# Kernel optimization log

Hardware: AMD Instinct MI355X
Metric: run time of the kernel (lower is better)

## Reference

```python
import jax, jax.numpy as jnp
import numpy as np

N = 50000          # total nodes
B = 10             # graphs in batch
NPG = N // B       # nodes per graph (equal-sized graphs)
E = 800000         # edges
IN_DIM = 128
HID = 128
NHEAD = 4
DHEAD = HID // NHEAD
T = 1000
SLOPE = 0.2        # leaky_relu negative slope
ALPHA_L = 2.0


def _ln(x, g=None, b=None, eps=1e-5):
    mu = jnp.mean(x, axis=-1, keepdims=True)
    var = jnp.var(x, axis=-1, keepdims=True)
    y = (x - mu) * jax.lax.rsqrt(var + eps)
    if g is not None:
        y = y * g + b
    return y


def _gatv2(h, src, dst, Ws, Wd, a, b):
    # DGL GATv2Conv, share_weights=False, residual=False, bias=True, activation=gelu
    fs = (h @ Ws).reshape(N, NHEAD, DHEAD)
    fd = (h @ Wd).reshape(N, NHEAD, DHEAD)
    # per-edge attention logits [E, NHEAD]
    e = jnp.sum(jax.nn.leaky_relu(fs[src] + fd[dst], SLOPE) * a, axis=-1)
    # edge softmax grouped by destination node
    m = jax.ops.segment_max(e, dst, num_segments=N)
    ee = jnp.exp(e - m[dst])
    den = jax.ops.segment_sum(ee, dst, num_segments=N)
    alpha = ee / den[dst]                                  # [E, NHEAD]
    rst = jax.ops.segment_sum(alpha[..., None] * fs[src], dst, num_segments=N)
    rst = jax.nn.gelu(rst + b.reshape(1, NHEAD, DHEAD), approximate=False)
    return rst.reshape(N, HID)


def _forward(x, noise, sab, somab, time_emb,
             Ws0, Wd0, a0, b0, g0, be0,
             Ws1, Wd1, a1, b1, g1, be1,
             Wo1, bo1, Wo2, bo2, src, dst, t):
    # sample_q: statistics-matched signed noise
    miu = jnp.mean(x, axis=0)
    std = jnp.std(x, axis=0, ddof=1)          # torch.std is unbiased
    nz = _ln(noise) * std + miu
    nz = jnp.sign(x) * jnp.abs(nz)
    s1 = jnp.repeat(sab[t], NPG)[:, None]
    s2 = jnp.repeat(somab[t], NPG)[:, None]
    x_t = s1 * x + s2 * nz
    temb = jnp.repeat(time_emb[t], NPG, axis=0)
    # Denoising_Unet
    h = jnp.concatenate([x_t, temb], axis=1)   # [N, IN_DIM+HID]
    h = _ln(_gatv2(h, src, dst, Ws0, Wd0, a0, b0), g0, be0)
    h_in = h
    h = _gatv2(h, src, dst, Ws1, Wd1, a1, b1)
    h = _ln(h + h_in, g1, be1)                 # residual (shapes match)
    out = jax.nn.relu(h @ Wo1 + bo1) @ Wo2 + bo2
    # loss_fn
    mse = jnp.mean((out - x) ** 2)
    on = out / jnp.maximum(jnp.linalg.norm(out, axis=-1, keepdims=True), 1e-12)
    xn = x / jnp.maximum(jnp.linalg.norm(x, axis=-1, keepdims=True), 1e-12)
    cos = jnp.mean((1.0 - jnp.sum(on * xn, axis=-1)) ** ALPHA_L)
    return mse + 0.1 * cos


def setup_inputs() -> dict:
    key = jax.random.key(0)
    ks = jax.random.split(key, 26)
    betas = np.linspace(1e-4, 0.02, T, dtype=np.float64)
    ab = np.cumprod(1.0 - betas)
    s = 0.02
    in0 = IN_DIM + HID
    inp = {}
    inp['x'] = jax.random.normal(ks[0], (N, IN_DIM), jnp.float32)
    inp['noise'] = jax.random.normal(ks[1], (N, IN_DIM), jnp.float32)
    inp['src'] = jax.random.randint(ks[2], (E,), 0, N, dtype=jnp.int32)
    inp['dst'] = jax.random.randint(ks[3], (E,), 0, N, dtype=jnp.int32)
    inp['t'] = jax.random.randint(ks[4], (B,), 0, T, dtype=jnp.int32)
    inp['sab'] = jnp.asarray(np.sqrt(ab), jnp.float32)
    inp['somab'] = jnp.asarray(np.sqrt(1.0 - ab), jnp.float32)
    inp['time_emb'] = jax.random.normal(ks[5], (T, HID), jnp.float32) * s
    inp['Ws0'] = jax.random.normal(ks[6], (in0, HID), jnp.float32) * s
    inp['Wd0'] = jax.random.normal(ks[7], (in0, HID), jnp.float32) * s
    inp['a0'] = jax.random.normal(ks[8], (NHEAD, DHEAD), jnp.float32) * s
    inp['b0'] = jnp.zeros((HID,), jnp.float32)
    inp['g0'] = jnp.ones((HID,), jnp.float32)
    inp['be0'] = jnp.zeros((HID,), jnp.float32)
    inp['Ws1'] = jax.random.normal(ks[9], (HID, HID), jnp.float32) * s
    inp['Wd1'] = jax.random.normal(ks[10], (HID, HID), jnp.float32) * s
    inp['a1'] = jax.random.normal(ks[11], (NHEAD, DHEAD), jnp.float32) * s
    inp['b1'] = jnp.zeros((HID,), jnp.float32)
    inp['g1'] = jnp.ones((HID,), jnp.float32)
    inp['be1'] = jnp.zeros((HID,), jnp.float32)
    inp['Wo1'] = jax.random.normal(ks[12], (HID, HID), jnp.float32) * s
    inp['bo1'] = jnp.zeros((HID,), jnp.float32)
    inp['Wo2'] = jax.random.normal(ks[13], (HID, IN_DIM), jnp.float32) * s
    inp['bo2'] = jnp.zeros((IN_DIM,), jnp.float32)
    return inp


def reference(x, noise, src, dst, t, sab, somab, time_emb,
              Ws0, Wd0, a0, b0, g0, be0,
              Ws1, Wd1, a1, b1, g1, be1,
              Wo1, bo1, Wo2, bo2):
    return _forward(x, noise, sab, somab, time_emb,
                    Ws0, Wd0, a0, b0, g0, be0,
                    Ws1, Wd1, a1, b1, g1, be1,
                    Wo1, bo1, Wo2, bo2, src, dst, t)
```

## Files before the change

### kernel.cpp

```cpp
#include <hip/hip_runtime.h>
#include <hip/hip_bf16.h>
#include <hip/hip_fp16.h>
#include <math.h>

#define NN 50000
#define EE 800000
#define NPG 5000

typedef short bf16x8 __attribute__((ext_vector_type(8)));
typedef float f32x4 __attribute__((ext_vector_type(4)));

__device__ __forceinline__ float gelu_exact(float v) {
    return 0.5f * v * (1.0f + erff(v * 0.70710678118654752440f));
}

__device__ __forceinline__ ushort f2b(float f) {
    union { float f; uint u; } v; v.f = f;
    uint r = (v.u + 0x7fffu + ((v.u >> 16) & 1)) >> 16;
    return (ushort)r;
}
__device__ __forceinline__ uint pack2(float a, float b) {
    return (uint)f2b(a) | ((uint)f2b(b) << 16);
}
__device__ __forceinline__ float blo(uint u) {
    union { uint u; float f; } v; v.u = u << 16; return v.f;
}
__device__ __forceinline__ float bhi(uint u) {
    union { uint u; float f; } v; v.u = u & 0xffff0000u; return v.f;
}
__device__ __forceinline__ void unpack8(uint4 u, float* f) {
    f[0] = blo(u.x); f[1] = bhi(u.x); f[2] = blo(u.y); f[3] = bhi(u.y);
    f[4] = blo(u.z); f[5] = bhi(u.z); f[6] = blo(u.w); f[7] = bhi(u.w);
}

__device__ __forceinline__ uchar f2e5m2(float v) {
    __half h = __float2half(v);
    union { __half h; ushort u; } c; c.h = h;
    return (uchar)((c.u + 0x7fu + ((c.u >> 8) & 1u)) >> 8);
}
__device__ __forceinline__ float e5m2f(uint b) {
    union { ushort u; __half h; } c; c.u = (ushort)(b << 8);
    return __half2float(c.h);
}
__device__ __forceinline__ void dec8(uint2 u, float* f) {
#pragma unroll
    for (int i = 0; i < 2; ++i) {
        uint w = (&u.x)[i];
        f[4 * i]     = e5m2f(w & 0xffu);
        f[4 * i + 1] = e5m2f((w >> 8) & 0xffu);
        f[4 * i + 2] = e5m2f((w >> 16) & 0xffu);
        f[4 * i + 3] = e5m2f((w >> 24) & 0xffu);
    }
}

__global__ __launch_bounds__(256) void head1_kernel(const float* __restrict__ x,
        float* __restrict__ sums, const int* __restrict__ dst, int* __restrict__ counts,
        const float* __restrict__ Ws0, const float* __restrict__ Wd0,
        const float* __restrict__ Ws1, const float* __restrict__ Wd1,
        const float* __restrict__ Wo1, const float* __restrict__ Wo2,
        ushort* __restrict__ Wt0, ushort* __restrict__ Wt1,
        ushort* __restrict__ Wo1t, ushort* __restrict__ Wo2t) {
    int bid = blockIdx.x;
    int tid = threadIdx.x;
    if (bid < 1024) {
        int col4 = (tid & 31) * 4;
        int rowgrp = tid >> 5;
        float s0 = 0.f, s1 = 0.f, s2 = 0.f, s3 = 0.f;
        float q0 = 0.f, q1 = 0.f, q2 = 0.f, q3 = 0.f;
        for (int r = bid * 8 + rowgrp; r < NN; r += 8192) {
            float4 v = *(const float4*)(x + (size_t)r * 128 + col4);
            s0 += v.x; s1 += v.y; s2 += v.z; s3 += v.w;
            q0 += v.x * v.x; q1 += v.y * v.y; q2 += v.z * v.z; q3 += v.w * v.w;
        }
        s0 += __shfl_xor(s0, 32); s1 += __shfl_xor(s1, 32);
        s2 += __shfl_xor(s2, 32); s3 += __shfl_xor(s3, 32);
        q0 += __shfl_xor(q0, 32); q1 += __shfl_xor(q1, 32);
        q2 += __shfl_xor(q2, 32); q3 += __shfl_xor(q3, 32);
        __shared__ float red[4][32][8];
        int wv = tid >> 6, l = tid & 63;
        if (l < 32) {
            float* p = red[wv][l];
            p[0] = s0; p[1] = s1; p[2] = s2; p[3] = s3;
            p[4] = q0; p[5] = q1; p[6] = q2; p[7] = q3;
        }
        __syncthreads();
        if (tid < 32) {
            float a0 = 0.f, a1 = 0.f, a2 = 0.f, a3 = 0.f;
            float b0 = 0.f, b1 = 0.f, b2 = 0.f, b3 = 0.f;
#pragma unroll
            for (int w = 0; w < 4; ++w) {
                float* p = red[w][tid];
                a0 += p[0]; a1 += p[1]; a2 += p[2]; a3 += p[3];
                b0 += p[4]; b1 += p[5]; b2 += p[6]; b3 += p[7];
            }
            int c = tid * 4;
            atomicAdd(&sums[c], a0); atomicAdd(&sums[c + 1], a1);
            atomicAdd(&sums[c + 2], a2); atomicAdd(&sums[c + 3], a3);
            atomicAdd(&sums[128 + c], b0); atomicAdd(&sums[128 + c + 1], b1);
            atomicAdd(&sums[128 + c + 2], b2); atomicAdd(&sums[128 + c + 3], b3);
        }
    } else if (bid < 4149) {
        int i = (bid - 1024) * 256 + tid;
        if (i < EE) atomicAdd(&counts[dst[i]], 1);
    } else {
        int i = (bid - 4149) * 256 + tid;
        if (i < 65536) {
            int c = i >> 8, k = i & 255;
            const float* W = (c < 128) ? Ws0 : Wd0;
            Wt0[c * 256 + k] = f2b(W[k * 128 + (c & 127)]);
        } else if (i < 98304) {
            int j = i - 65536;
            int c = j >> 7, k = j & 127;
            const float* W = (c < 128) ? Ws1 : Wd1;
            Wt1[c * 128 + k] = f2b(W[k * 128 + (c & 127)]);
        } else if (i < 114688) {
            int j = i - 98304;
            int c = j >> 7, k = j & 127;
            Wo1t[c * 128 + k] = f2b(Wo1[k * 128 + c]);
        } else if (i < 131072) {
            int j = i - 114688;
            int c = j >> 7, k = j & 127;
            Wo2t[c * 128 + k] = f2b(Wo2[k * 128 + c]);
        }
    }
}

__global__ __launch_bounds__(1024) void head2_kernel(const int* __restrict__ counts,
        int* __restrict__ blockSums, float* __restrict__ stats, int n) {
    int bid = blockIdx.x;
    int tid = threadIdx.x;
    if (bid < 49) {
        int i = bid * 1024 + tid;
        int v = (i < n) ? counts[i] : 0;
#pragma unroll
        for (int o = 32; o > 0; o >>= 1) v += __shfl_down(v, o);
        __shared__ int sh[16];
        int lane = tid & 63, wv = tid >> 6;
        if (lane == 0) sh[wv] = v;
        __syncthreads();
        if (tid == 0) {
            int s = 0;
#pragma unroll
            for (int k = 0; k < 16; ++k) s += sh[k];
            blockSums[bid] = s;
        }
    } else {
        if (tid < 128) {
            int c = tid;
            float sum = stats[c], sumsq = stats[128 + c];
            float mu = sum / (float)n;
            float var = (sumsq - sum * sum / (float)n) / (float)(n - 1);
            stats[256 + c] = mu;
            stats[384 + c] = sqrtf(fmaxf(var, 0.f));
        }
    }
}

__global__ __launch_bounds__(1024) void head3_kernel(const float* __restrict__ x,
        const float* __restrict__ noise, const int* __restrict__ t,
        const float* __restrict__ sab, const float* __restrict__ somab,
        const float* __restrict__ temb, const float* __restrict__ stats,
        ushort* __restrict__ h,
        const int* __restrict__ counts, const int* __restrict__ blockSums,
        int* __restrict__ indptr, int* __restrict__ cursor, int n) {
    int bid = blockIdx.x;
    int tid = threadIdx.x;
    if (bid < 3125) {
        int wid = bid * 16 + (tid >> 6);
        int lane = tid & 63;
        int tt = t[wid / NPG];
        float s1 = sab[tt], s2v = somab[tt];
        float2 nz = ((const float2*)noise)[(size_t)wid * 64 + lane];
        float s = nz.x + nz.y;
        float sq = nz.x * nz.x + nz.y * nz.y;
#pragma unroll
        for (int o = 1; o < 64; o <<= 1) { s += __shfl_xor(s, o); sq += __shfl_xor(sq, o); }
        float mu = s * (1.f / 128.f);
        float var = sq * (1.f / 128.f) - mu * mu;
        float r = rsqrtf(var + 1e-5f);
        int f0 = 2 * lane, f1 = f0 + 1;
        float y0 = (nz.x - mu) * r * stats[384 + f0] + stats[256 + f0];
        float y1 = (nz.y - mu) * r * stats[384 + f1] + stats[256 + f1];
        float2 xv = ((const float2*)x)[(size_t)wid * 64 + lane];
        float sg0 = (xv.x > 0.f) ? 1.f : ((xv.x < 0.f) ? -1.f : 0.f);
        float sg1 = (xv.y > 0.f) ? 1.f : ((xv.y < 0.f) ? -1.f : 0.f);
        float n0 = sg0 * fabsf(y0);
        float n1 = sg1 * fabsf(y1);
        float xt0 = s1 * xv.x + s2v * n0;
        float xt1 = s1 * xv.y + s2v * n1;
        uint* row = (uint*)(h + (size_t)wid * 256);
        row[lane] = pack2(xt0, xt1);
        float2 te = ((const float2*)(temb + (size_t)tt * 128))[lane];
        row[64 + lane] = pack2(te.x, te.y);
    } else {
        int b = bid - 3125;
        __shared__ int sOff, sTot;
        if (tid < 64) {
            int v = (tid < 49) ? blockSums[tid] : 0;
            int incl = v;
#pragma unroll
            for (int o = 1; o < 64; o <<= 1) {
                int tv = __shfl_up(incl, o);
                if ((tid & 63) >= o) incl += tv;
            }
            int off = (b == 0) ? 0 : __shfl(incl, b - 1);
            int tot = __shfl(incl, 48);
            if (tid == 0) { sOff = off; sTot = tot; }
        }
        __syncthreads();
        int i = b * 1024 + tid;
        int v = (i < n) ? counts[i] : 0;
        int lane = tid & 63, wv = tid >> 6;
        int incl = v;
#pragma unroll
        for (int o = 1; o < 64; o <<= 1) {
            int tv = __shfl_up(incl, o);
            if (lane >= o) incl += tv;
        }
        __shared__ int wsum[16];
        __shared__ int woff[16];
        if (lane == 63) wsum[wv] = incl;
        __syncthreads();
        if (tid == 0) {
            int s = 0;
#pragma unroll
            for (int k = 0; k < 16; ++k) { woff[k] = s; s += wsum[k]; }
        }
        __syncthreads();
        int ex = incl - v + woff[wv] + sOff;
        if (i < n) { indptr[i] = ex; cursor[i] = ex; }
        if (b == 48 && tid == 0) indptr[n] = sTot;
    }
}

__global__ __launch_bounds__(1024) void scatter_kernel(const int* __restrict__ src,
        const int* __restrict__ dst, int* __restrict__ cursor,
        int* __restrict__ csr_src, int e) {
    int i = blockIdx.x * 1024 + threadIdx.x;
    if (i < e) {
        int p = atomicAdd(&cursor[dst[i]], 1);
        csr_src[p] = src[i];
    }
}

template<int K, int NCOL, int EPI>
__global__ __launch_bounds__(256, 2) void mfma_gemm(const ushort* __restrict__ A,
        const ushort* __restrict__ Wt, const float* __restrict__ bias,
        uchar* __restrict__ C8, ushort* __restrict__ C1,
        const float* __restrict__ X, float* __restrict__ lossAcc, int M) {
    constexpr int NFRAG = NCOL / 16;
    constexpr int KSTEPS = K / 32;
    __shared__ ushort Bs[32 * NCOL];
    int tid = threadIdx.x;
    int wave = tid >> 6, lane = tid & 63;
    int l15 = lane & 15, g = lane >> 4;
    int rowBase = blockIdx.x * 64 + wave * 16;
    int rc = min(rowBase + l15, M - 1);
    const ushort* Arow = A + (size_t)rc * K + g * 8;

    f32x4 acc[NFRAG] = {};

    for (int ks = 0; ks < KSTEPS; ++ks) {
#pragma unroll
        for (int i = 0; i < NCOL / 64; ++i) {
            int ch = tid + i * 256;
            int c = ch >> 2, q = ch & 3;
            float4 v = *(const float4*)(Wt + (size_t)c * K + ks * 32 + q * 8);
            int off = c * 64 + ((q * 16) ^ ((c & 7) << 4));
            *(float4*)((char*)Bs + off) = v;
        }
        __syncthreads();
        bf16x8 af = *(const bf16x8*)(Arow + ks * 32);
        int roff = l15 * 64 + ((g * 16) ^ ((l15 & 7) << 4));
#pragma unroll
        for (int n = 0; n < NFRAG; ++n) {
            bf16x8 bf = *(const bf16x8*)((const char*)Bs + n * 1024 + roff);
            acc[n] = __builtin_amdgcn_mfma_f32_16x16x32_bf16(af, bf, acc[n], 0, 0, 0);
        }
        __syncthreads();
    }

    if (EPI != 3) {
#pragma unroll
        for (int n = 0; n < NFRAG; ++n) {
            int col = n * 16 + l15;
#pragma unroll
            for (int j = 0; j < 4; ++j) {
                int row = rowBase + g * 4 + j;
                if (row < M) {
                    float v = acc[n][j];
                    if (EPI == 1) v = fmaxf(v + bias[col], 0.f);
                    if (NCOL == 256) {
                        if (n < 8) C8[(size_t)row * 128 + col] = f2e5m2(v);
                        else       C1[(size_t)row * 128 + col - 128] = f2b(v);
                    } else {
                        C1[(size_t)row * 128 + col] = f2b(v);
                    }
                }
            }
        }
    } else {
        float td2 = 0.f, tcl = 0.f;
#pragma unroll
        for (int j = 0; j < 4; ++j) {
            int row = rowBase + g * 4 + j;
            bool rv = row < M;
            float d2 = 0.f, oo = 0.f, xx = 0.f, ox = 0.f;
#pragma unroll
            for (int n = 0; n < NFRAG; ++n) {
                int col = n * 16 + l15;
                float o = rv ? (acc[n][j] + bias[col]) : 0.f;
                float xv = rv ? X[(size_t)row * 128 + col] : 0.f;
                float e = o - xv;
                d2 += e * e; oo += o * o; xx += xv * xv; ox += o * xv;
            }
#pragma unroll
            for (int off = 1; off < 16; off <<= 1) {
                d2 += __shfl_xor(d2, off); oo += __shfl_xor(oo, off);
                xx += __shfl_xor(xx, off); ox += __shfl_xor(ox, off);
            }
            if (rv) {
                float no = fmaxf(sqrtf(oo), 1e-12f);
                float nx = fmaxf(sqrtf(xx), 1e-12f);
                float cs = 1.f - ox / (no * nx);
                td2 += d2; tcl += cs * cs;
            }
        }
        __shared__ float sd2[16], scl[16];
        if (l15 == 0) { sd2[wave * 4 + g] = td2; scl[wave * 4 + g] = tcl; }
        __syncthreads();
        if (tid == 0) {
            float a2 = 0.f, ac = 0.f;
#pragma unroll
            for (int k2 = 0; k2 < 16; ++k2) { a2 += sd2[k2]; ac += scl[k2]; }
            atomicAdd(&lossAcc[0], a2);
            atomicAdd(&lossAcc[1], ac);
        }
    }
}

__global__ __launch_bounds__(256) void gat_ln_kernel(const uchar* __restrict__ fs8,
        const ushort* __restrict__ fd, const float* __restrict__ a,
        const float* __restrict__ bias, const int* __restrict__ indptr,
        const int* __restrict__ csr_src, const ushort* __restrict__ residB,
        const float* __restrict__ g, const float* __restrict__ be,
        ushort* __restrict__ outB, int n) {
    int wid = (blockIdx.x * blockDim.x + threadIdx.x) >> 6;
    int lane = threadIdx.x & 63;
    if (wid >= n) return;
    int quad = lane >> 4, s = lane & 15;
    int beg = indptr[wid], cnt = indptr[wid + 1] - beg;
    const int* ip = csr_src + beg;
    const uint2* fs2 = (const uint2*)fs8;

    uint4 fdq = ((const uint4*)fd)[(size_t)wid * 16 + s];
    float fdv[8]; unpack8(fdq, fdv);
    float av[8];
    {
        float4 a0 = *(const float4*)(a + 8 * s);
        float4 a1 = *(const float4*)(a + 8 * s + 4);
        av[0] = a0.x; av[1] = a0.y; av[2] = a0.z; av[3] = a0.w;
        av[4] = a1.x; av[5] = a1.y; av[6] = a1.z; av[7] = a1.w;
    }

    int i0 = (quad < cnt) ? ip[quad] : 0;
    int i1 = (4 + quad < cnt) ? ip[4 + quad] : 0;
    uint2 vA = fs2[(size_t)i0 * 16 + s];
    uint2 vB = fs2[(size_t)i1 * 16 + s];
    int p0 = (8  < cnt) ? ip[8]  : 0;
    int p1 = (9  < cnt) ? ip[9]  : 0;
    int p2 = (10 < cnt) ? ip[10] : 0;
    int p3 = (11 < cnt) ? ip[11] : 0;

    float den = 0.f;
    float acc[8] = {};
    for (int j = 0; j < cnt; j += 4) {
        uint2 cur = vA; vA = vB;
        int pe = (quad == 0) ? p0 : (quad == 1) ? p1 : (quad == 2) ? p2 : p3;
        vB = fs2[(size_t)pe * 16 + s];
        p0 = (j + 12 < cnt) ? ip[j + 12] : 0;
        p1 = (j + 13 < cnt) ? ip[j + 13] : 0;
        p2 = (j + 14 < cnt) ? ip[j + 14] : 0;
        p3 = (j + 15 < cnt) ? ip[j + 15] : 0;
        float c[8]; dec8(cur, c);
        float p = 0.f;
#pragma unroll
        for (int i = 0; i < 8; ++i) {
            float tv = c[i] + fdv[i];
            tv = (tv > 0.f) ? tv : 0.2f * tv;
            p = fmaf(tv, av[i], p);
        }
        p += __shfl_xor(p, 1);
        p += __shfl_xor(p, 2);
        float w = (j + quad < cnt) ? __expf(p) : 0.f;
        den += w;
#pragma unroll
        for (int i = 0; i < 8; ++i) acc[i] = fmaf(w, c[i], acc[i]);
    }
#pragma unroll
    for (int i = 0; i < 8; ++i) {
        acc[i] += __shfl_xor(acc[i], 16);
        acc[i] += __shfl_xor(acc[i], 32);
    }
    den += __shfl_xor(den, 16);
    den += __shfl_xor(den, 32);
    float inv = (cnt > 0) ? 1.f / den : 0.f;

    float bi[8];
    {
        float4 b0v = *(const float4*)(bias + 8 * s);
        float4 b1v = *(const float4*)(bias + 8 * s + 4);
        bi[0] = b0v.x; bi[1] = b0v.y; bi[2] = b0v.z; bi[3] = b0v.w;
        bi[4] = b1v.x; bi[5] = b1v.y; bi[6] = b1v.z; bi[7] = b1v.w;
    }
    float r[8];
#pragma unroll
    for (int i = 0; i < 8; ++i) r[i] = gelu_exact(acc[i] * inv + bi[i]);
    if (residB) {
        uint4 rq = ((const uint4*)residB)[(size_t)wid * 16 + s];
        float rv[8]; unpack8(rq, rv);
#pragma unroll
        for (int i = 0; i < 8; ++i) r[i] += rv[i];
    }
    float ssum = 0.f, ssq = 0.f;
#pragma unroll
    for (int i = 0; i < 8; ++i) { ssum += r[i]; ssq += r[i] * r[i]; }
#pragma unroll
    for (int o = 1; o < 16; o <<= 1) { ssum += __shfl_xor(ssum, o); ssq += __shfl_xor(ssq, o); }
    float mu = ssum * (1.f / 128.f);
    float var = ssq * (1.f / 128.f) - mu * mu;
    float rstd = rsqrtf(var + 1e-5f);
    float gv[8], bv[8];
    {
        float4 g0v = *(const float4*)(g + 8 * s);
        float4 g1v = *(const float4*)(g + 8 * s + 4);
        gv[0] = g0v.x; gv[1] = g0v.y; gv[2] = g0v.z; gv[3] = g0v.w;
        gv[4] = g1v.x; gv[5] = g1v.y; gv[6] = g1v.z; gv[7] = g1v.w;
        float4 e0v = *(const float4*)(be + 8 * s);
        float4 e1v = *(const float4*)(be + 8 * s + 4);
        bv[0] = e0v.x; bv[1] = e0v.y; bv[2] = e0v.z; bv[3] = e0v.w;
        bv[4] = e1v.x; bv[5] = e1v.y; bv[6] = e1v.z; bv[7] = e1v.w;
    }
    float o_[8];
#pragma unroll
    for (int i = 0; i < 8; ++i) o_[i] = (r[i] - mu) * rstd * gv[i] + bv[i];
    if (quad == 0) {
        uint4 w4;
        w4.x = pack2(o_[0], o_[1]); w4.y = pack2(o_[2], o_[3]);
        w4.z = pack2(o_[4], o_[5]); w4.w = pack2(o_[6], o_[7]);
        ((uint4*)outB)[(size_t)wid * 16 + s] = w4;
    }
}

__global__ void loss_final2(const float* __restrict__ lossAcc, float* __restrict__ outp, int n) {
    outp[0] = lossAcc[0] / ((float)n * 128.f) + 0.1f * (lossAcc[1] / (float)n);
}

extern "C" void kernel_launch(void* const* d_in, const int* in_sizes, int n_in,
                              void* d_out, int out_size, void* d_ws, size_t ws_size,
                              hipStream_t stream) {
    const int N = NN, E = EE;
    const float* x     = (const float*)d_in[0];
    const float* noise = (const float*)d_in[1];
    const int*   src   = (const int*)d_in[2];
    const int*   dst   = (const int*)d_in[3];
    const int*   t     = (const int*)d_in[4];
    const float* sab   = (const float*)d_in[5];
    const float* somab = (const float*)d_in[6];
    const float* temb  = (const float*)d_in[7];
    const float* Ws0   = (const float*)d_in[8];
    const float* Wd0   = (const float*)d_in[9];
    const float* a0    = (const float*)d_in[10];
    const float* b0    = (const float*)d_in[11];
    const float* g0    = (const float*)d_in[12];
    const float* be0   = (const float*)d_in[13];
    const float* Ws1   = (const float*)d_in[14];
    const float* Wd1   = (const float*)d_in[15];
    const float* a1    = (const float*)d_in[16];
    const float* b1    = (const float*)d_in[17];
    const float* g1    = (const float*)d_in[18];
    const float* be1   = (const float*)d_in[19];
    const float* Wo1   = (const float*)d_in[20];
    const float* bo1   = (const float*)d_in[21];
    const float* Wo2   = (const float*)d_in[22];
    const float* bo2   = (const float*)d_in[23];

    float* ws = (float*)d_ws;
    ushort* hB  = (ushort*)ws;
    ushort* Pb  = (ushort*)ws;
    uchar*  fs8 = (uchar*)(ws + (size_t)N * 128);
    ushort* z   = (ushort*)(ws + (size_t)N * 128);
    ushort* fdB = (ushort*)(ws + (size_t)N * 192);
    ushort* Qb  = fdB;
    float* wtail = ws + (size_t)N * 384;
    ushort* Wt0  = (ushort*)wtail;
    ushort* Wt1  = (ushort*)(wtail + 32768);
    ushort* Wo1t = (ushort*)(wtail + 49152);
    ushort* Wo2t = (ushort*)(wtail + 57344);
    float* stats    = wtail + 65536;
    float* lossAcc  = stats + 512;
    int* counts  = (int*)(lossAcc + 2048);
    int* indptr  = counts + N;
    int* cursor  = indptr + N + 1;
    int* csr_src = cursor + N;
    int* blockSums = csr_src + E;

    hipMemsetAsync(stats, 0, 514 * sizeof(float), stream);
    hipMemsetAsync(counts, 0, (size_t)N * sizeof(int), stream);

    head1_kernel<<<4661, 256, 0, stream>>>(x, stats, dst, counts,
                                           Ws0, Wd0, Ws1, Wd1, Wo1, Wo2,
                                           Wt0, Wt1, Wo1t, Wo2t);
    head2_kernel<<<50, 1024, 0, stream>>>(counts, blockSums, stats, N);
    head3_kernel<<<3174, 1024, 0, stream>>>(x, noise, t, sab, somab, temb, stats, hB,
                                            counts, blockSums, indptr, cursor, N);
    scatter_kernel<<<(E + 1023) / 1024, 1024, 0, stream>>>(src, dst, cursor, csr_src, E);

    int gemmGrid = (N + 63) / 64;
    mfma_gemm<256, 256, 0><<<gemmGrid, 256, 0, stream>>>(hB, Wt0, nullptr, fs8, fdB,
                                                         nullptr, nullptr, N);
    gat_ln_kernel<<<(N + 3) / 4, 256, 0, stream>>>(fs8, fdB, a0, b0, indptr, csr_src,
                                                   nullptr, g0, be0, Pb, N);
    mfma_gemm<128, 256, 0><<<gemmGrid, 256, 0, stream>>>(Pb, Wt1, nullptr, fs8, fdB,
                                                         nullptr, nullptr, N);
    gat_ln_kernel<<<(N + 3) / 4, 256, 0, stream>>>(fs8, fdB, a1, b1, indptr, csr_src,
                                                   Pb, g1, be1, Qb, N);
    mfma_gemm<128, 128, 1><<<gemmGrid, 256, 0, stream>>>(Qb, Wo1t, bo1, nullptr, z,
                                                         nullptr, nullptr, N);
    mfma_gemm<128, 128, 3><<<gemmGrid, 256, 0, stream>>>(z, Wo2t, bo2, nullptr, nullptr,
                                                         x, lossAcc, N);
    loss_final2<<<1, 1, 0, stream>>>(lossAcc, (float*)d_out, N);
}
```

Before: 395.6 us.

## Fuse head stages, merge scatter into first GEMM, fuse MLP and loss

Removes head2 by having each block compute the column stats itself and redo the prefix offset sum directly from counts. The edge scatter is merged into the first GEMM launch as extra blocks, so the two run in one grid. The two output MLP GEMMs and the loss are fused into one kernel that keeps the intermediate activations and both weight matrices in LDS. The two memsets are merged into one. This cuts kernel launches and the global round trip of z, at the cost of redundant prefix summing per block and 80KB of LDS per block in the MLP kernel, which lowers occupancy.

```diff
diff --git a/kernel.cpp b/kernel.cpp
--- a/kernel.cpp
+++ b/kernel.cpp
@@ -125,47 +125,24 @@
     }
 }
 
-__global__ __launch_bounds__(1024) void head2_kernel(const int* __restrict__ counts,
-        int* __restrict__ blockSums, float* __restrict__ stats, int n) {
-    int bid = blockIdx.x;
-    int tid = threadIdx.x;
-    if (bid < 49) {
-        int i = bid * 1024 + tid;
-        int v = (i < n) ? counts[i] : 0;
-#pragma unroll
-        for (int o = 32; o > 0; o >>= 1) v += __shfl_down(v, o);
-        __shared__ int sh[16];
-        int lane = tid & 63, wv = tid >> 6;
-        if (lane == 0) sh[wv] = v;
-        __syncthreads();
-        if (tid == 0) {
-            int s = 0;
-#pragma unroll
-            for (int k = 0; k < 16; ++k) s += sh[k];
-            blockSums[bid] = s;
-        }
-    } else {
-        if (tid < 128) {
-            int c = tid;
-            float sum = stats[c], sumsq = stats[128 + c];
-            float mu = sum / (float)n;
-            float var = (sumsq - sum * sum / (float)n) / (float)(n - 1);
-            stats[256 + c] = mu;
-            stats[384 + c] = sqrtf(fmaxf(var, 0.f));
-        }
-    }
-}
-
 __global__ __launch_bounds__(1024) void head3_kernel(const float* __restrict__ x,
         const float* __restrict__ noise, const int* __restrict__ t,
         const float* __restrict__ sab, const float* __restrict__ somab,
         const float* __restrict__ temb, const float* __restrict__ stats,
-        ushort* __restrict__ h,
-        const int* __restrict__ counts, const int* __restrict__ blockSums,
+        ushort* __restrict__ h, const int* __restrict__ counts,
         int* __restrict__ indptr, int* __restrict__ cursor, int n) {
     int bid = blockIdx.x;
     int tid = threadIdx.x;
     if (bid < 3125) {
+        __shared__ float smu[128], sstd[128];
+        if (tid < 128) {
+            float sum = stats[tid], sumsq = stats[128 + tid];
+            float mu = sum / (float)n;
+            float var = (sumsq - sum * sum / (float)n) / (float)(n - 1);
+            smu[tid] = mu;
+            sstd[tid] = sqrtf(fmaxf(var, 0.f));
+        }
+        __syncthreads();
         int wid = bid * 16 + (tid >> 6);
         int lane = tid & 63;
         int tt = t[wid / NPG];
@@ -179,8 +156,8 @@
         float var = sq * (1.f / 128.f) - mu * mu;
         float r = rsqrtf(var + 1e-5f);
         int f0 = 2 * lane, f1 = f0 + 1;
-        float y0 = (nz.x - mu) * r * stats[384 + f0] + stats[256 + f0];
-        float y1 = (nz.y - mu) * r * stats[384 + f1] + stats[256 + f1];
+        float y0 = (nz.x - mu) * r * sstd[f0] + smu[f0];
+        float y1 = (nz.y - mu) * r * sstd[f1] + smu[f1];
         float2 xv = ((const float2*)x)[(size_t)wid * 64 + lane];
         float sg0 = (xv.x > 0.f) ? 1.f : ((xv.x < 0.f) ? -1.f : 0.f);
         float sg1 = (xv.y > 0.f) ? 1.f : ((xv.y < 0.f) ? -1.f : 0.f);
@@ -194,23 +171,26 @@
         row[64 + lane] = pack2(te.x, te.y);
     } else {
         int b = bid - 3125;
-        __shared__ int sOff, sTot;
-        if (tid < 64) {
-            int v = (tid < 49) ? blockSums[tid] : 0;
-            int incl = v;
-#pragma unroll
-            for (int o = 1; o < 64; o <<= 1) {
-                int tv = __shfl_up(incl, o);
-                if ((tid & 63) >= o) incl += tv;
-            }
-            int off = (b == 0) ? 0 : __shfl(incl, b - 1);
-            int tot = __shfl(incl, 48);
-            if (tid == 0) { sOff = off; sTot = tot; }
-        }
-        __syncthreads();
-        int i = b * 1024 + tid;
+        int base = b * 1024;
+        int accp = 0;
+        for (int i = tid; i < base; i += 1024) accp += counts[i];
+#pragma unroll
+        for (int o = 32; o > 0; o >>= 1) accp += __shfl_down(accp, o);
+        __shared__ int offW[16];
+        __shared__ int sOffS;
+        int lane = tid & 63, wv = tid >> 6;
+        if (lane == 0) offW[wv] = accp;
+        __syncthreads();
+        if (tid == 0) {
+            int sum = 0;
+#pragma unroll
+            for (int k = 0; k < 16; ++k) sum += offW[k];
+            sOffS = sum;
+        }
+        __syncthreads();
+        int sOff = sOffS;
+        int i = base + tid;
         int v = (i < n) ? counts[i] : 0;
-        int lane = tid & 63, wv = tid >> 6;
         int incl = v;
 #pragma unroll
         for (int o = 1; o < 64; o <<= 1) {
@@ -221,36 +201,81 @@
         __shared__ int woff[16];
         if (lane == 63) wsum[wv] = incl;
         __syncthreads();
+        __shared__ int blkTotS;
         if (tid == 0) {
-            int s = 0;
-#pragma unroll
-            for (int k = 0; k < 16; ++k) { woff[k] = s; s += wsum[k]; }
+            int sum = 0;
+#pragma unroll
+            for (int k = 0; k < 16; ++k) { woff[k] = sum; sum += wsum[k]; }
+            blkTotS = sum;
         }
         __syncthreads();
         int ex = incl - v + woff[wv] + sOff;
         if (i < n) { indptr[i] = ex; cursor[i] = ex; }
-        if (b == 48 && tid == 0) indptr[n] = sTot;
-    }
-}
-
-__global__ __launch_bounds__(1024) void scatter_kernel(const int* __restrict__ src,
-        const int* __restrict__ dst, int* __restrict__ cursor,
-        int* __restrict__ csr_src, int e) {
-    int i = blockIdx.x * 1024 + threadIdx.x;
-    if (i < e) {
-        int p = atomicAdd(&cursor[dst[i]], 1);
-        csr_src[p] = src[i];
-    }
-}
-
-template<int K, int NCOL, int EPI>
-__global__ __launch_bounds__(256, 2) void mfma_gemm(const ushort* __restrict__ A,
-        const ushort* __restrict__ Wt, const float* __restrict__ bias,
-        uchar* __restrict__ C8, ushort* __restrict__ C1,
-        const float* __restrict__ X, float* __restrict__ lossAcc, int M) {
-    constexpr int NFRAG = NCOL / 16;
-    constexpr int KSTEPS = K / 32;
-    __shared__ ushort Bs[32 * NCOL];
+        if (b == 48 && tid == 0) indptr[n] = sOff + blkTotS;
+    }
+}
+
+__global__ __launch_bounds__(256, 2) void gemm_scatter_kernel(const ushort* __restrict__ A,
+        const ushort* __restrict__ Wt, uchar* __restrict__ C8, ushort* __restrict__ C1,
+        const int* __restrict__ src, const int* __restrict__ dst,
+        int* __restrict__ cursor, int* __restrict__ csr_src, int GG, int M) {
+    __shared__ ushort Bs[32 * 256];
+    int tid = threadIdx.x;
+    if ((int)blockIdx.x >= GG) {
+        int i = ((int)blockIdx.x - GG) * 256 + tid;
+        if (i < EE) {
+            int p = atomicAdd(&cursor[dst[i]], 1);
+            csr_src[p] = src[i];
+        }
+        return;
+    }
+    constexpr int K = 256;
+    int wave = tid >> 6, lane = tid & 63;
+    int l15 = lane & 15, g = lane >> 4;
+    int rowBase = blockIdx.x * 64 + wave * 16;
+    int rc = min(rowBase + l15, M - 1);
+    const ushort* Arow = A + (size_t)rc * K + g * 8;
+
+    f32x4 acc[16] = {};
+    for (int ks = 0; ks < K / 32; ++ks) {
+#pragma unroll
+        for (int i = 0; i < 4; ++i) {
+            int ch = tid + i * 256;
+            int c = ch >> 2, q = ch & 3;
+            float4 v = *(const float4*)(Wt + (size_t)c * K + ks * 32 + q * 8);
+            int off = c * 64 + ((q * 16) ^ ((c & 7) << 4));
+            *(float4*)((char*)Bs + off) = v;
+        }
+        __syncthreads();
+        bf16x8 af = *(const bf16x8*)(Arow + ks * 32);
+        int roff = l15 * 64 + ((g * 16) ^ ((l15 & 7) << 4));
+#pragma unroll
+        for (int n = 0; n < 16; ++n) {
+            bf16x8 bf = *(const bf16x8*)((const char*)Bs + n * 1024 + roff);
+            acc[n] = __builtin_amdgcn_mfma_f32_16x16x32_bf16(af, bf, acc[n], 0, 0, 0);
+        }
+        __syncthreads();
+    }
+#pragma unroll
+    for (int n = 0; n < 16; ++n) {
+        int col = n * 16 + l15;
+#pragma unroll
+        for (int j = 0; j < 4; ++j) {
+            int row = rowBase + g * 4 + j;
+            if (row < M) {
+                float v = acc[n][j];
+                if (n < 8) C8[(size_t)row * 128 + col] = f2e5m2(v);
+                else       C1[(size_t)row * 128 + col - 128] = f2b(v);
+            }
+        }
+    }
+}
+
+__global__ __launch_bounds__(256, 2) void mfma_gemm1(const ushort* __restrict__ A,
+        const ushort* __restrict__ Wt, uchar* __restrict__ C8,
+        ushort* __restrict__ C1, int M) {
+    constexpr int K = 128;
+    __shared__ ushort Bs[32 * 256];
     int tid = threadIdx.x;
     int wave = tid >> 6, lane = tid & 63;
     int l15 = lane & 15, g = lane >> 4;
@@ -258,11 +283,10 @@
     int rc = min(rowBase + l15, M - 1);
     const ushort* Arow = A + (size_t)rc * K + g * 8;
 
-    f32x4 acc[NFRAG] = {};
-
-    for (int ks = 0; ks < KSTEPS; ++ks) {
-#pragma unroll
-        for (int i = 0; i < NCOL / 64; ++i) {
+    f32x4 acc[16] = {};
+    for (int ks = 0; ks < K / 32; ++ks) {
+#pragma unroll
+        for (int i = 0; i < 4; ++i) {
             int ch = tid + i * 256;
             int c = ch >> 2, q = ch & 3;
             float4 v = *(const float4*)(Wt + (size_t)c * K + ks * 32 + q * 8);
@@ -273,68 +297,23 @@
         bf16x8 af = *(const bf16x8*)(Arow + ks * 32);
         int roff = l15 * 64 + ((g * 16) ^ ((l15 & 7) << 4));
 #pragma unroll
-        for (int n = 0; n < NFRAG; ++n) {
+        for (int n = 0; n < 16; ++n) {
             bf16x8 bf = *(const bf16x8*)((const char*)Bs + n * 1024 + roff);
             acc[n] = __builtin_amdgcn_mfma_f32_16x16x32_bf16(af, bf, acc[n], 0, 0, 0);
         }
         __syncthreads();
     }
-
-    if (EPI != 3) {
-#pragma unroll
-        for (int n = 0; n < NFRAG; ++n) {
-            int col = n * 16 + l15;
-#pragma unroll
-            for (int j = 0; j < 4; ++j) {
-                int row = rowBase + g * 4 + j;
-                if (row < M) {
-                    float v = acc[n][j];
-                    if (EPI == 1) v = fmaxf(v + bias[col], 0.f);
-                    if (NCOL == 256) {
-                        if (n < 8) C8[(size_t)row * 128 + col] = f2e5m2(v);
-                        else       C1[(size_t)row * 128 + col - 128] = f2b(v);
-                    } else {
-                        C1[(size_t)row * 128 + col] = f2b(v);
-                    }
-                }
-            }
-        }
-    } else {
-        float td2 = 0.f, tcl = 0.f;
+#pragma unroll
+    for (int n = 0; n < 16; ++n) {
+        int col = n * 16 + l15;
 #pragma unroll
         for (int j = 0; j < 4; ++j) {
             int row = rowBase + g * 4 + j;
-            bool rv = row < M;
-            float d2 = 0.f, oo = 0.f, xx = 0.f, ox = 0.f;
-#pragma unroll
-            for (int n = 0; n < NFRAG; ++n) {
-                int col = n * 16 + l15;
-                float o = rv ? (acc[n][j] + bias[col]) : 0.f;
-                float xv = rv ? X[(size_t)row * 128 + col] : 0.f;
-                float e = o - xv;
-                d2 += e * e; oo += o * o; xx += xv * xv; ox += o * xv;
+            if (row < M) {
+                float v = acc[n][j];
+                if (n < 8) C8[(size_t)row * 128 + col] = f2e5m2(v);
+                else       C1[(size_t)row * 128 + col - 128] = f2b(v);
             }
-#pragma unroll
-            for (int off = 1; off < 16; off <<= 1) {
-                d2 += __shfl_xor(d2, off); oo += __shfl_xor(oo, off);
-                xx += __shfl_xor(xx, off); ox += __shfl_xor(ox, off);
-            }
-            if (rv) {
-                float no = fmaxf(sqrtf(oo), 1e-12f);
-                float nx = fmaxf(sqrtf(xx), 1e-12f);
-                float cs = 1.f - ox / (no * nx);
-                td2 += d2; tcl += cs * cs;
-            }
-        }
-        __shared__ float sd2[16], scl[16];
-        if (l15 == 0) { sd2[wave * 4 + g] = td2; scl[wave * 4 + g] = tcl; }
-        __syncthreads();
-        if (tid == 0) {
-            float a2 = 0.f, ac = 0.f;
-#pragma unroll
-            for (int k2 = 0; k2 < 16; ++k2) { a2 += sd2[k2]; ac += scl[k2]; }
-            atomicAdd(&lossAcc[0], a2);
-            atomicAdd(&lossAcc[1], ac);
         }
     }
 }
@@ -449,6 +428,105 @@
         w4.x = pack2(o_[0], o_[1]); w4.y = pack2(o_[2], o_[3]);
         w4.z = pack2(o_[4], o_[5]); w4.w = pack2(o_[6], o_[7]);
         ((uint4*)outB)[(size_t)wid * 16 + s] = w4;
+    }
+}
+
+__global__ __launch_bounds__(256, 2) void mlp_loss_kernel(const ushort* __restrict__ Qb,
+        const ushort* __restrict__ Wo1t, const ushort* __restrict__ Wo2t,
+        const float* __restrict__ bo1, const float* __restrict__ bo2,
+        const float* __restrict__ X, float* __restrict__ lossAcc, int M) {
+    __shared__ ushort W1[16384];
+    __shared__ ushort W2[16384];
+    __shared__ ushort Zt[8192];
+    int tid = threadIdx.x;
+    int wave = tid >> 6, lane = tid & 63;
+    int l15 = lane & 15, g = lane >> 4;
+#pragma unroll
+    for (int it = 0; it < 8; ++it) {
+        int q = (it * 256 + tid) * 16;
+        int col = q >> 8, qk = q & 255;
+        int srcb = (col << 8) + (qk ^ ((col & 7) << 4));
+        *(float4*)((char*)W1 + q) = *(const float4*)((const char*)Wo1t + srcb);
+        *(float4*)((char*)W2 + q) = *(const float4*)((const char*)Wo2t + srcb);
+    }
+    int rowBase = blockIdx.x * 64 + wave * 16;
+    int rc = min(rowBase + l15, M - 1);
+    const ushort* Arow = Qb + (size_t)rc * 128 + g * 8;
+    f32x4 acc1[8] = {};
+    __syncthreads();
+#pragma unroll
+    for (int ks = 0; ks < 4; ++ks) {
+        bf16x8 af = *(const bf16x8*)(Arow + ks * 32);
+#pragma unroll
+        for (int n = 0; n < 8; ++n) {
+            int col = n * 16 + l15;
+            int boff = (col << 8) + ((ks * 64 + g * 16) ^ ((col & 7) << 4));
+            bf16x8 bf = *(const bf16x8*)((const char*)W1 + boff);
+            acc1[n] = __builtin_amdgcn_mfma_f32_16x16x32_bf16(af, bf, acc1[n], 0, 0, 0);
+        }
+    }
+#pragma unroll
+    for (int n = 0; n < 8; ++n) {
+        int col = n * 16 + l15;
+        float bv = bo1[col];
+#pragma unroll
+        for (int j = 0; j < 4; ++j) {
+            int lr = wave * 16 + g * 4 + j;
+            float v = fmaxf(acc1[n][j] + bv, 0.f);
+            int zoff = (lr << 8) + ((col * 2) ^ ((lr & 7) << 4));
+            *(ushort*)((char*)Zt + zoff) = f2b(v);
+        }
+    }
+    __syncthreads();
+    f32x4 acc2[8] = {};
+    int lr = wave * 16 + l15;
+#pragma unroll
+    for (int ks = 0; ks < 4; ++ks) {
+        int aoff = (lr << 8) + ((ks * 64 + g * 16) ^ ((lr & 7) << 4));
+        bf16x8 af = *(const bf16x8*)((const char*)Zt + aoff);
+#pragma unroll
+        for (int n = 0; n < 8; ++n) {
+            int col = n * 16 + l15;
+            int boff = (col << 8) + ((ks * 64 + g * 16) ^ ((col & 7) << 4));
+            bf16x8 bf = *(const bf16x8*)((const char*)W2 + boff);
+            acc2[n] = __builtin_amdgcn_mfma_f32_16x16x32_bf16(af, bf, acc2[n], 0, 0, 0);
+        }
+    }
+    float td2 = 0.f, tcl = 0.f;
+#pragma unroll
+    for (int j = 0; j < 4; ++j) {
+        int row = rowBase + g * 4 + j;
+        bool rv = row < M;
+        float d2 = 0.f, oo = 0.f, xx = 0.f, ox = 0.f;
+#pragma unroll
+        for (int n = 0; n < 8; ++n) {
+            int col = n * 16 + l15;
+            float ov = rv ? (acc2[n][j] + bo2[col]) : 0.f;
+            float xv = rv ? X[(size_t)row * 128 + col] : 0.f;
+            float e = ov - xv;
+            d2 += e * e; oo += ov * ov; xx += xv * xv; ox += ov * xv;
+        }
+#pragma unroll
+        for (int off = 1; off < 16; off <<= 1) {
+            d2 += __shfl_xor(d2, off); oo += __shfl_xor(oo, off);
+            xx += __shfl_xor(xx, off); ox += __shfl_xor(ox, off);
+        }
+        if (rv) {
+            float no = fmaxf(sqrtf(oo), 1e-12f);
+            float nx = fmaxf(sqrtf(xx), 1e-12f);
+            float cs = 1.f - ox / (no * nx);
+            td2 += d2; tcl += cs * cs;
+        }
+    }
+    __shared__ float sd2[16], scl[16];
+    if (l15 == 0) { sd2[wave * 4 + g] = td2; scl[wave * 4 + g] = tcl; }
+    __syncthreads();
+    if (tid == 0) {
+        float a2 = 0.f, ac = 0.f;
+#pragma unroll
+        for (int k2 = 0; k2 < 16; ++k2) { a2 += sd2[k2]; ac += scl[k2]; }
+        atomicAdd(&lossAcc[0], a2);
+        atomicAdd(&lossAcc[1], ac);
     }
 }
 
@@ -489,7 +567,6 @@
     ushort* hB  = (ushort*)ws;
     ushort* Pb  = (ushort*)ws;
     uchar*  fs8 = (uchar*)(ws + (size_t)N * 128);
-    ushort* z   = (ushort*)(ws + (size_t)N * 128);
     ushort* fdB = (ushort*)(ws + (size_t)N * 192);
     ushort* Qb  = fdB;
     float* wtail = ws + (size_t)N * 384;
@@ -499,35 +576,28 @@
     ushort* Wo2t = (ushort*)(wtail + 57344);
     float* stats    = wtail + 65536;
     float* lossAcc  = stats + 512;
-    int* counts  = (int*)(lossAcc + 2048);
+    int* counts  = (int*)(lossAcc + 2);
     int* indptr  = counts + N;
     int* cursor  = indptr + N + 1;
     int* csr_src = cursor + N;
-    int* blockSums = csr_src + E;
-
-    hipMemsetAsync(stats, 0, 514 * sizeof(float), stream);
-    hipMemsetAsync(counts, 0, (size_t)N * sizeof(int), stream);
+
+    hipMemsetAsync(stats, 0, (size_t)(514 + N) * sizeof(float), stream);
 
     head1_kernel<<<4661, 256, 0, stream>>>(x, stats, dst, counts,
                                            Ws0, Wd0, Ws1, Wd1, Wo1, Wo2,
                                            Wt0, Wt1, Wo1t, Wo2t);
-    head2_kernel<<<50, 1024, 0, stream>>>(counts, blockSums, stats, N);
     head3_kernel<<<3174, 1024, 0, stream>>>(x, noise, t, sab, somab, temb, stats, hB,
-                                            counts, blockSums, indptr, cursor, N);
-    scatter_kernel<<<(E + 1023) / 1024, 1024, 0, stream>>>(src, dst, cursor, csr_src, E);
+                                            counts, indptr, cursor, N);
 
     int gemmGrid = (N + 63) / 64;
-    mfma_gemm<256, 256, 0><<<gemmGrid, 256, 0, stream>>>(hB, Wt0, nullptr, fs8, fdB,
-                                                         nullptr, nullptr, N);
+    gemm_scatter_kernel<<<gemmGrid + 3125, 256, 0, stream>>>(hB, Wt0, fs8, fdB,
+                                                             src, dst, cursor, csr_src,
+                                                             gemmGrid, N);
     gat_ln_kernel<<<(N + 3) / 4, 256, 0, stream>>>(fs8, fdB, a0, b0, indptr, csr_src,
                                                    nullptr, g0, be0, Pb, N);
-    mfma_gemm<128, 256, 0><<<gemmGrid, 256, 0, stream>>>(Pb, Wt1, nullptr, fs8, fdB,
-                                                         nullptr, nullptr, N);
+    mfma_gemm1<<<gemmGrid, 256, 0, stream>>>(Pb, Wt1, fs8, fdB, N);
     gat_ln_kernel<<<(N + 3) / 4, 256, 0, stream>>>(fs8, fdB, a1, b1, indptr, csr_src,
                                                    Pb, g1, be1, Qb, N);
-    mfma_gemm<128, 128, 1><<<gemmGrid, 256, 0, stream>>>(Qb, Wo1t, bo1, nullptr, z,
-                                                         nullptr, nullptr, N);
-    mfma_gemm<128, 128, 3><<<gemmGrid, 256, 0, stream>>>(z, Wo2t, bo2, nullptr, nullptr,
-                                                         x, lossAcc, N);
+    mlp_loss_kernel<<<gemmGrid, 256, 0, stream>>>(Qb, Wo1t, Wo2t, bo1, bo2, x, lossAcc, N);
     loss_final2<<<1, 1, 0, stream>>>(lossAcc, (float*)d_out, N);
 }
```

Result: slower. 403.9 us (+2.1%).
